# Performance work log

Hardware: AMD Instinct MI355X
Metric: run time of the kernel (lower is better)

The kernel has to match this reference:

```python
import jax, jax.numpy as jnp
import numpy as np

K = 5            # Chebyshev order (hard-coded in ManEmbedder conv_kwargs)
LAMBDA_MAX = 3.0 # fixed lambda_max from init
N_NODES = 100000
N_EDGES = 400000
N_GRAPHS = 64
H1, H2 = 128, 512


def _seg_sum(vals, idx, n):
    return jax.ops.segment_sum(vals, idx, num_segments=n)


def _cheb_edge_weights(edge_index, n_nodes):
    """Scaled Laplacian L_hat = 2*(I - D^-1/2 A D^-1/2)/lambda_max - I as edge weights.
    Matches PyG get_laplacian('sym') + ChebConv.__norm__ with fixed lambda_max.
    Degrees are computed at row = edge_index[0] (as in get_laplacian)."""
    row, col = edge_index[0], edge_index[1]
    ones = jnp.ones(row.shape[0], jnp.float32)
    deg = _seg_sum(ones, row, n_nodes)
    dinv = jnp.where(deg > 0, jax.lax.rsqrt(jnp.maximum(deg, 1e-12)), 0.0)
    w_edge = -(dinv[row] * dinv[col]) * (2.0 / LAMBDA_MAX)  # off-diagonal of L_hat
    w_loop = 2.0 / LAMBDA_MAX - 1.0                          # diagonal of L_hat (scalar)
    return w_edge, w_loop


def cheb_conv(x, edge_index, W, b, reverse):
    """PyG ChebConv. flow='target_to_source' (reverse=False): aggregate at row, gather at col.
    reverse=True flips the propagation direction (source_to_target)."""
    n = x.shape[0]
    w_edge, w_loop = _cheb_edge_weights(edge_index, n)
    row, col = edge_index[0], edge_index[1]
    src, dst = (row, col) if reverse else (col, row)

    def prop(h):  # L_hat @ h via gather-scale-scatter + diagonal term
        return _seg_sum(w_edge[:, None] * h[src], dst, n) + w_loop * h

    tx0 = x
    out = tx0 @ W[0]
    tx1 = prop(tx0)
    out = out + tx1 @ W[1]
    for k in range(2, K):
        tx2 = 2.0 * prop(tx1) - tx0
        out = out + tx2 @ W[k]
        tx0, tx1 = tx1, tx2
    return out + b


def bidir_block(x, edge_index, Wf, bf, Wb, bb):
    # Bidirectional: one ChebConv per edge direction, outputs summed.
    return cheb_conv(x, edge_index, Wf, bf, False) + cheb_conv(x, edge_index, Wb, bb, True)


def setup_inputs() -> dict:
    key = jax.random.key(0)
    ks = jax.random.split(key, 12)
    x = jax.random.normal(ks[0], (N_NODES, 1), jnp.float32)
    edge_index = jax.random.randint(ks[1], (2, N_EDGES), 0, N_NODES, dtype=jnp.int64)
    batch = jnp.sort(jax.random.randint(ks[2], (N_NODES,), 0, N_GRAPHS, dtype=jnp.int64))

    def glorot(k, shape):
        fan_in, fan_out = shape[-2], shape[-1]
        s = (6.0 / (fan_in + fan_out)) ** 0.5
        return jax.random.uniform(k, shape, jnp.float32, -s, s)

    return {
        "x": x, "edge_index": edge_index, "batch": batch,
        "W1f": glorot(ks[3], (K, 1, H1)),  "b1f": jnp.zeros((H1,), jnp.float32),
        "W1b": glorot(ks[4], (K, 1, H1)),  "b1b": jnp.zeros((H1,), jnp.float32),
        "W2f": glorot(ks[5], (K, H1, H2)), "b2f": jnp.zeros((H2,), jnp.float32),
        "W2b": glorot(ks[6], (K, H1, H2)), "b2b": jnp.zeros((H2,), jnp.float32),
    }


def reference(x, edge_index, batch, W1f, b1f, W1b, b1b, W2f, b2f, W2b, b2b):
    h = jax.nn.relu(bidir_block(x, edge_index, W1f, b1f, W1b, b1b))
    h = jax.nn.relu(bidir_block(h, edge_index, W2f, b2f, W2b, b2b))
    # global mean pool over batch index -> [N_GRAPHS, 512]
    summed = _seg_sum(h, batch, N_GRAPHS)
    counts = _seg_sum(jnp.ones((h.shape[0],), jnp.float32), batch, N_GRAPHS)
    return summed / jnp.maximum(counts, 1.0)[:, None]
```

## Files before the change

kernel.cpp:

```cpp
#include <hip/hip_runtime.h>
#include <hip/hip_bf16.h>

typedef unsigned short u16;
typedef unsigned int u32;
typedef __attribute__((ext_vector_type(4))) float f32x4;
typedef __attribute__((ext_vector_type(8))) short bf16x8;

struct __align__(8) ew_t { int s; float w; };

#define WLOOP (2.0f/3.0f - 1.0f)
#define WEDGE (-(2.0f/3.0f))

__device__ __forceinline__ float bf2f(u16 h){ u32 u = ((u32)h)<<16; float f; __builtin_memcpy(&f,&u,4); return f; }
__device__ __forceinline__ u16 f2bf(float f){ u32 u; __builtin_memcpy(&u,&f,4); u32 r = u + 0x7fffu + ((u>>16)&1u); return (u16)(r>>16); }

__device__ __forceinline__ void async16(u16* lds, const u16* g){
  __builtin_amdgcn_global_load_lds((const __attribute__((address_space(1))) u32*)g,
                                   (__attribute__((address_space(3))) u32*)lds, 16, 0, 0);
}

__global__ void k_hist(const int* __restrict__ ei, int E, int* cntf, int* cntb){
  int e = blockIdx.x*256 + threadIdx.x; if (e>=E) return;
  atomicAdd(&cntf[ei[e]],1); atomicAdd(&cntb[ei[E+e]],1);
}
__global__ void k_dinv(const int* __restrict__ cntf, float* dinv, int N){
  int n = blockIdx.x*256+threadIdx.x; if(n>=N) return;
  int d = cntf[n]; dinv[n] = d>0 ? rsqrtf((float)d) : 0.f;
}
__global__ void k_scanA(const int* __restrict__ cnt, int* excl, int* bsum, int n){
  __shared__ int sh[256]; int i = blockIdx.x*256+threadIdx.x;
  int v = (i<n)? cnt[i]:0; sh[threadIdx.x]=v; __syncthreads();
  for (int off=1; off<256; off<<=1){
    int t = (threadIdx.x>=off)? sh[threadIdx.x-off]:0; __syncthreads();
    sh[threadIdx.x]+=t; __syncthreads();
  }
  if (i<n) excl[i]=sh[threadIdx.x]-v;
  if (threadIdx.x==255) bsum[blockIdx.x]=sh[255];
}
__global__ void k_scanB(int* bsum, int nb, int* total){
  __shared__ int sh[512]; int t = threadIdx.x;
  int v = (t<nb)? bsum[t]:0; sh[t]=v; __syncthreads();
  for(int off=1; off<512; off<<=1){
    int a = (t>=off)? sh[t-off]:0; __syncthreads();
    sh[t]+=a; __syncthreads();
  }
  if (t<nb) bsum[t]=sh[t]-v;
  if (t==511) *total = sh[511];
}
__global__ void k_scanC(int* excl, const int* __restrict__ bsum, int n, int* cur){
  int i = blockIdx.x*256+threadIdx.x; if(i>=n) return;
  int v = excl[i]+bsum[blockIdx.x]; excl[i]=v; cur[i]=v;
}
__global__ void k_fill(const int* __restrict__ ei, int E, const float* __restrict__ dinv,
                       int* curf, int* curb, ew_t* ewf, ew_t* ewb){
  int e = blockIdx.x*256+threadIdx.x; if(e>=E) return;
  int r = ei[e], c = ei[E+e];
  float w = WEDGE * dinv[r]*dinv[c];
  int pf = atomicAdd(&curf[r],1); ewf[pf] = {c, w};
  int pb = atomicAdd(&curb[c],1); ewb[pb] = {r, w};
}

__global__ void k_sprop(const float* __restrict__ t1f, const float* __restrict__ t0f, float* df,
                        const float* __restrict__ t1b, const float* __restrict__ t0b, float* db,
                        const int* __restrict__ offf, const ew_t* __restrict__ ewfa,
                        const int* __restrict__ offb, const ew_t* __restrict__ ewba,
                        int N){
  int i = blockIdx.x*256+threadIdx.x;
  int dir = 0; if (i >= N){ i -= N; dir = 1; }
  if (i >= N) return;
  const float* t1; const float* t0; float* d; const int* off; const ew_t* ew;
  if (dir==0){ t1=t1f; t0=t0f; d=df; off=offf; ew=ewfa; }
  else       { t1=t1b; t0=t0b; d=db; off=offb; ew=ewba; }
  float a = WLOOP * t1[i];
  int e = off[i], e1 = off[i+1];
  for (; e+4<=e1; e+=4){
    ew_t p0=ew[e], p1=ew[e+1], p2=ew[e+2], p3=ew[e+3];
    float v0=t1[p0.s], v1=t1[p1.s], v2=t1[p2.s], v3=t1[p3.s];
    a += p0.w*v0 + p1.w*v1 + p2.w*v2 + p3.w*v3;
  }
  for (; e<e1; ++e){ ew_t p=ew[e]; a += p.w*t1[p.s]; }
  d[i] = t0 ? (2.f*a - t0[i]) : a;
}

__global__ void k_expand(const float* __restrict__ x,
   const float* __restrict__ cf1, const float* __restrict__ cf2, const float* __restrict__ cf3, const float* __restrict__ cf4,
   const float* __restrict__ cb1, const float* __restrict__ cb2, const float* __restrict__ cb3, const float* __restrict__ cb4,
   const float* __restrict__ W1f, const float* __restrict__ b1f,
   const float* __restrict__ W1b, const float* __restrict__ b1b,
   u16* __restrict__ T, int N){
  __shared__ float swf[640], swb[640], sbias[128];
  int tid = threadIdx.x;
  for (int i=tid;i<640;i+=256){ swf[i]=W1f[i]; swb[i]=W1b[i]; }
  if (tid<128) sbias[tid]=b1f[tid]+b1b[tid];
  __syncthreads();
  int j = tid & 127; int n = blockIdx.x*2 + (tid>>7);
  if (n>=N) return;
  float xx = x[n];
  float acc = sbias[j] + xx*(swf[j]+swb[j]);
  acc += cf1[n]*swf[128+j]; acc += cf2[n]*swf[256+j]; acc += cf3[n]*swf[384+j]; acc += cf4[n]*swf[512+j];
  acc += cb1[n]*swb[128+j]; acc += cb2[n]*swb[256+j]; acc += cb3[n]*swb[384+j]; acc += cb4[n]*swb[512+j];
  T[(size_t)n*1152 + j] = f2bf(fmaxf(acc,0.f));
}

__global__ void k_vprop(u16* __restrict__ T,
   const int* __restrict__ offf, const ew_t* __restrict__ ewfa,
   const int* __restrict__ offb, const ew_t* __restrict__ ewba,
   int ssf, int dsf, int psf, int ssb, int dsb, int psb, int N){
  int gid = blockIdx.x*256 + threadIdx.x;
  int wid = gid>>6, l = threadIdx.x & 63;
  int dir = 0; if (wid >= N){ wid -= N; dir = 1; }
  if (wid >= N) return;
  const int* off; const ew_t* ew; int ss,ds,ps;
  if (!dir){ off=offf;ew=ewfa;ss=ssf;ds=dsf;ps=psf; }
  else     { off=offb;ew=ewba;ss=ssb;ds=dsb;ps=psb; }
  const u16* Tss = T + (size_t)ss*128 + 2*l;
  u32 u = *(const u32*)(Tss + (size_t)wid*1152);
  float a0 = WLOOP*bf2f(u&0xffff), a1 = WLOOP*bf2f(u>>16);
  int e = off[wid], e1 = off[wid+1];
  for (; e+4<=e1; e+=4){
    ew_t p0=ew[e], p1=ew[e+1], p2=ew[e+2], p3=ew[e+3];
    u32 g0 = *(const u32*)(Tss + (size_t)p0.s*1152);
    u32 g1 = *(const u32*)(Tss + (size_t)p1.s*1152);
    u32 g2 = *(const u32*)(Tss + (size_t)p2.s*1152);
    u32 g3 = *(const u32*)(Tss + (size_t)p3.s*1152);
    a0 += p0.w*bf2f(g0&0xffff) + p1.w*bf2f(g1&0xffff) + p2.w*bf2f(g2&0xffff) + p3.w*bf2f(g3&0xffff);
    a1 += p0.w*bf2f(g0>>16)    + p1.w*bf2f(g1>>16)    + p2.w*bf2f(g2>>16)    + p3.w*bf2f(g3>>16);
  }
  for (; e<e1; ++e){
    ew_t p = ew[e];
    u32 ug = *(const u32*)(Tss + (size_t)p.s*1152);
    a0 += p.w*bf2f(ug&0xffff); a1 += p.w*bf2f(ug>>16);
  }
  float r0=a0, r1=a1;
  if (ps >= 0){
    u32 up = *(const u32*)(T + ((size_t)wid*1152 + ps*128) + 2*l);
    r0 = 2.f*a0 - bf2f(up&0xffff); r1 = 2.f*a1 - bf2f(up>>16);
  }
  *(u32*)(T + ((size_t)wid*1152 + ds*128) + 2*l) = ((u32)f2bf(r1)<<16) | (u32)f2bf(r0);
}

__global__ void k_wprep(const float* __restrict__ W2f, const float* __restrict__ W2b,
                        const float* __restrict__ b2f, const float* __restrict__ b2b,
                        u16* __restrict__ Wt2, float* __restrict__ bias2){
  int i = blockIdx.x*256+threadIdx.x;
  if (i < 512) bias2[i] = b2f[i]+b2b[i];
  if (i >= 512*1152) return;
  int j = i&7, l = (i>>3)&63, nt = (i>>9)&31, t = i>>14;
  int col = nt*16 + (l&15);
  int k   = t*32 + (l>>4)*8 + j;
  int s2 = k>>7, c = k&127;
  float v;
  if (s2==0)      v = W2f[c*512+col] + W2b[c*512+col];
  else if (s2<5)  v = W2f[(s2*128+c)*512 + col];
  else            v = W2b[((s2-4)*128+c)*512 + col];
  Wt2[i] = f2bf(v);
}

__global__ __launch_bounds__(512, 4) void k_gemm(const u16* __restrict__ T, const u16* __restrict__ Wt2,
                        const float* __restrict__ bias2, const int* __restrict__ batch,
                        float* __restrict__ outp, int Mvalid, int NB){
  int bid = blockIdx.x;
  int r8 = bid & 7, q = bid >> 3;
  int bn = q & 1, bm = (q >> 1)*8 + r8;
  if (bm >= NB) return;
  __shared__ u16 Al[2][128*32];
  int tid = threadIdx.x, w = tid>>6, l = tid&63;
  int wr = w>>2, wc = w&3;
  int hi = l>>4, lo = l&15;

  f32x4 acc[4][4];
  #pragma unroll
  for (int m=0;m<4;m++)
    #pragma unroll
    for (int n=0;n<4;n++){ acc[m][n][0]=0.f; acc[m][n][1]=0.f; acc[m][n][2]=0.f; acc[m][n][3]=0.f; }

  int sr = tid>>2, sp = tid&3;
  int csrc = ((sp ^ ((sr>>1)&3)))*8;
  const u16* asrc = T + (size_t)(bm*128 + sr)*1152 + csrc;
  const int adst = tid*8;
  int rsw = (hi ^ ((lo>>1)&3))*8;
  const int abase = (wr*64 + lo)*32 + rsw;
  const u16* bsrc = Wt2 + ((size_t)(bn*16 + wc*4)*64 + l)*8;

  #define LOADB(dst, t_) do { \
    _Pragma("unroll") \
    for (int n_=0;n_<4;n_++) dst[n_] = *(const bf16x8*)(bsrc + (size_t)(t_)*16384 + n_*512); \
  } while(0)

  bf16x8 be[4], bo[4];
  async16(&Al[0][adst], asrc);
  LOADB(be, 0);

  for (int t=0; t<36; t+=2){
    if (t < 35){
      async16(&Al[1][adst], asrc + (t+1)*32);
      LOADB(bo, t+1);
      asm volatile("s_waitcnt vmcnt(5)" ::: "memory");
    } else {
      asm volatile("s_waitcnt vmcnt(0)" ::: "memory");
    }
    asm volatile("s_barrier" ::: "memory");
    __builtin_amdgcn_s_setprio(1);
    #pragma unroll
    for (int m=0;m<4;m++){
      bf16x8 af = *(const bf16x8*)&Al[0][abase + m*512];
      #pragma unroll
      for (int n=0;n<4;n++)
        acc[m][n] = __builtin_amdgcn_mfma_f32_16x16x32_bf16(af, be[n], acc[m][n], 0, 0, 0);
    }
    __builtin_amdgcn_s_setprio(0);
    asm volatile("s_barrier" ::: "memory");
    if (t+2 < 36){
      async16(&Al[0][adst], asrc + (t+2)*32);
      LOADB(be, t+2);
      asm volatile("s_waitcnt vmcnt(5)" ::: "memory");
    } else {
      asm volatile("s_waitcnt vmcnt(0)" ::: "memory");
    }
    asm volatile("s_barrier" ::: "memory");
    __builtin_amdgcn_s_setprio(1);
    #pragma unroll
    for (int m=0;m<4;m++){
      bf16x8 af = *(const bf16x8*)&Al[1][abase + m*512];
      #pragma unroll
      for (int n=0;n<4;n++)
        acc[m][n] = __builtin_amdgcn_mfma_f32_16x16x32_bf16(af, bo[n], acc[m][n], 0, 0, 0);
    }
    __builtin_amdgcn_s_setprio(0);
    asm volatile("s_barrier" ::: "memory");
  }
  #undef LOADB

  int bg[16];
  #pragma unroll
  for (int m=0;m<4;m++)
    #pragma unroll
    for (int j2=0;j2<4;j2++){
      int row = bm*128 + wr*64 + m*16 + hi*4 + j2;
      bg[m*4+j2] = (row < Mvalid) ? batch[row] : -1;
    }
  #pragma unroll
  for (int n=0;n<4;n++){
    int col = bn*256 + wc*64 + n*16 + lo;
    float bc = bias2[col];
    int cg2 = -1; float ssum = 0.f;
    #pragma unroll
    for (int idx=0; idx<16; idx++){
      int g = bg[idx];
      if (g >= 0){
        float val = fmaxf(acc[idx>>2][n][idx&3] + bc, 0.f);
        if (g != cg2){ if (cg2 >= 0) atomicAdd(&outp[(cg2<<9) + col], ssum); cg2 = g; ssum = 0.f; }
        ssum += val;
      }
    }
    if (cg2 >= 0) atomicAdd(&outp[(cg2<<9) + col], ssum);
  }
}

__global__ void k_count(const int* __restrict__ batch, int* cg, int N){
  __shared__ int sh[64];
  int t = threadIdx.x;
  if (t < 64) sh[t] = 0;
  __syncthreads();
  int base = blockIdx.x*1024;
  #pragma unroll
  for (int i = base + t; i < base + 1024; i += 256){
    if (i < N) atomicAdd(&sh[batch[i]], 1);
  }
  __syncthreads();
  if (t < 64){ int v = sh[t]; if (v) atomicAdd(&cg[t], v); }
}

__global__ void k_div(float* out, const int* __restrict__ cg, int total){
  int i = blockIdx.x*256+threadIdx.x; if (i>=total) return;
  int g = i>>9; out[i] /= fmaxf((float)cg[g], 1.f);
}

extern "C" void kernel_launch(void* const* d_in, const int* in_sizes, int n_in,
                              void* d_out, int out_size, void* d_ws, size_t ws_size,
                              hipStream_t stream) {
  const float* x   = (const float*)d_in[0];
  const int*   ei  = (const int*)d_in[1];
  const int*   bat = (const int*)d_in[2];
  const float* W1f = (const float*)d_in[3];
  const float* b1f = (const float*)d_in[4];
  const float* W1b = (const float*)d_in[5];
  const float* b1b = (const float*)d_in[6];
  const float* W2f = (const float*)d_in[7];
  const float* b2f = (const float*)d_in[8];
  const float* W2b = (const float*)d_in[9];
  const float* b2b = (const float*)d_in[10];

  const int N  = in_sizes[0];
  const int E  = in_sizes[1] / 2;
  const int NP = ((N + 127)/128)*128;
  const int NB = NP/128;

  size_t p = 0;
  auto A = [&](size_t sz){ size_t r = p; p += (sz + 255) & ~(size_t)255; return r; };
  size_t o_cnt  = A(2*(size_t)N*4);
  size_t o_offf = A(((size_t)N+1)*4);
  size_t o_offb = A(((size_t)N+1)*4);
  size_t o_curf = A((size_t)N*4);
  size_t o_curb = A((size_t)N*4);
  size_t o_bsum = A(512*4);
  size_t o_dinv = A((size_t)N*4);
  size_t o_ewf  = A((size_t)E*8);
  size_t o_ewb  = A((size_t)E*8);
  size_t o_cf   = A(8*(size_t)N*4);
  size_t o_Wt   = A((size_t)512*1152*2);
  size_t o_b2   = A(512*4);
  size_t o_cg   = A(64*4);
  size_t o_T    = A((size_t)NP*1152*2);
  if (p > ws_size) return;

  char* ws = (char*)d_ws;
  int*   cnt_f = (int*)(ws + o_cnt);
  int*   cnt_b = cnt_f + N;
  int*   off_f = (int*)(ws + o_offf);
  int*   off_b = (int*)(ws + o_offb);
  int*   cur_f = (int*)(ws + o_curf);
  int*   cur_b = (int*)(ws + o_curb);
  int*   bsum  = (int*)(ws + o_bsum);
  float* dinv  = (float*)(ws + o_dinv);
  ew_t*  ewf   = (ew_t*)(ws + o_ewf);
  ew_t*  ewb   = (ew_t*)(ws + o_ewb);
  float* cf1   = (float*)(ws + o_cf);
  float* cf2   = cf1 + N; float* cf3 = cf2 + N; float* cf4 = cf3 + N;
  float* cb1   = cf4 + N; float* cb2 = cb1 + N; float* cb3 = cb2 + N; float* cb4 = cb3 + N;
  u16*   Wt2   = (u16*)(ws + o_Wt);
  float* bias2 = (float*)(ws + o_b2);
  int*   cg    = (int*)(ws + o_cg);
  u16*   T     = (u16*)(ws + o_T);
  float* outp  = (float*)d_out;

  const int nbN = (N + 255)/256;
  const int nbE = (E + 255)/256;
  const int nb2N = (2*N + 255)/256;

  hipMemsetAsync(cnt_f, 0, 2*(size_t)N*4, stream);
  hipMemsetAsync(cg, 0, 64*4, stream);
  hipMemsetAsync(d_out, 0, (size_t)out_size*4, stream);
  if (NP > N) hipMemsetAsync(T + (size_t)N*1152, 0, (size_t)(NP-N)*1152*2, stream);

  k_hist<<<nbE,256,0,stream>>>(ei, E, cnt_f, cnt_b);
  k_dinv<<<nbN,256,0,stream>>>(cnt_f, dinv, N);
  k_scanA<<<nbN,256,0,stream>>>(cnt_f, off_f, bsum, N);
  k_scanB<<<1,512,0,stream>>>(bsum, nbN, off_f + N);
  k_scanC<<<nbN,256,0,stream>>>(off_f, bsum, N, cur_f);
  k_scanA<<<nbN,256,0,stream>>>(cnt_b, off_b, bsum, N);
  k_scanB<<<1,512,0,stream>>>(bsum, nbN, off_b + N);
  k_scanC<<<nbN,256,0,stream>>>(off_b, bsum, N, cur_b);
  k_fill<<<nbE,256,0,stream>>>(ei, E, dinv, cur_f, cur_b, ewf, ewb);

  k_sprop<<<nb2N,256,0,stream>>>(x,   nullptr, cf1,  x,   nullptr, cb1, off_f,ewf, off_b,ewb, N);
  k_sprop<<<nb2N,256,0,stream>>>(cf1, x,       cf2,  cb1, x,       cb2, off_f,ewf, off_b,ewb, N);
  k_sprop<<<nb2N,256,0,stream>>>(cf2, cf1,     cf3,  cb2, cb1,     cb3, off_f,ewf, off_b,ewb, N);
  k_sprop<<<nb2N,256,0,stream>>>(cf3, cf2,     cf4,  cb3, cb2,     cb4, off_f,ewf, off_b,ewb, N);
  k_expand<<<(N+1)/2,256,0,stream>>>(x, cf1,cf2,cf3,cf4, cb1,cb2,cb3,cb4, W1f,b1f,W1b,b1b, T, N);

  k_wprep<<<(512*1152+255)/256,256,0,stream>>>(W2f, W2b, b2f, b2b, Wt2, bias2);

  const int vb = (2*N*64 + 255)/256;
  k_vprop<<<vb,256,0,stream>>>(T, off_f,ewf, off_b,ewb, 0,1,-1, 0,5,-1, N);
  k_vprop<<<vb,256,0,stream>>>(T, off_f,ewf, off_b,ewb, 1,2, 0, 5,6, 0, N);
  k_vprop<<<vb,256,0,stream>>>(T, off_f,ewf, off_b,ewb, 2,3, 1, 6,7, 5, N);
  k_vprop<<<vb,256,0,stream>>>(T, off_f,ewf, off_b,ewb, 3,4, 2, 7,8, 6, N);

  k_count<<<(N+1023)/1024,256,0,stream>>>(bat, cg, N);
  const int gemmGrid = ((NB + 7)/8)*8*2;
  k_gemm<<<gemmGrid,512,0,stream>>>(T, Wt2, bias2, bat, outp, N, NB);
  k_div<<<(out_size+255)/256,256,0,stream>>>(outp, cg, out_size);
}
```

Before: 639.8 us.

## Triple-buffer GEMM A tiles and predicate-unroll sparse propagation loops by eight

The GEMM main loop moves from a two-stage LDS ring to a three-stage ring, issuing the A-tile async load two steps ahead and the B register loads one step ahead, so each step needs one fewer wait on global memory. The scalar and vector sparse propagation kernels replace the 4-way unroll plus remainder loop with an 8-way unrolled loop whose tail lanes are masked by clamping the index and zeroing the weight. This puts more gathers in flight per node and removes the remainder loop, at the cost of redundant loads for masked lanes. The larger LDS footprint may lower GEMM occupancy.

Measured after the change: 700.9 us. 9.6% more time.

```diff
diff --git a/kernel.cpp b/kernel.cpp
--- a/kernel.cpp
+++ b/kernel.cpp
@@ -73,12 +73,14 @@
   else       { t1=t1b; t0=t0b; d=db; off=offb; ew=ewba; }
   float a = WLOOP * t1[i];
   int e = off[i], e1 = off[i+1];
-  for (; e+4<=e1; e+=4){
-    ew_t p0=ew[e], p1=ew[e+1], p2=ew[e+2], p3=ew[e+3];
-    float v0=t1[p0.s], v1=t1[p1.s], v2=t1[p2.s], v3=t1[p3.s];
-    a += p0.w*v0 + p1.w*v1 + p2.w*v2 + p3.w*v3;
-  }
-  for (; e<e1; ++e){ ew_t p=ew[e]; a += p.w*t1[p.s]; }
+  for (; e < e1; e += 8){
+    #pragma unroll
+    for (int j=0;j<8;j++){
+      int idx = e + j; bool v = idx < e1;
+      ew_t p = ew[v ? idx : e1-1];
+      a += (v ? p.w : 0.f) * t1[p.s];
+    }
+  }
   d[i] = t0 ? (2.f*a - t0[i]) : a;
 }
 
@@ -117,19 +119,16 @@
   u32 u = *(const u32*)(Tss + (size_t)wid*1152);
   float a0 = WLOOP*bf2f(u&0xffff), a1 = WLOOP*bf2f(u>>16);
   int e = off[wid], e1 = off[wid+1];
-  for (; e+4<=e1; e+=4){
-    ew_t p0=ew[e], p1=ew[e+1], p2=ew[e+2], p3=ew[e+3];
-    u32 g0 = *(const u32*)(Tss + (size_t)p0.s*1152);
-    u32 g1 = *(const u32*)(Tss + (size_t)p1.s*1152);
-    u32 g2 = *(const u32*)(Tss + (size_t)p2.s*1152);
-    u32 g3 = *(const u32*)(Tss + (size_t)p3.s*1152);
-    a0 += p0.w*bf2f(g0&0xffff) + p1.w*bf2f(g1&0xffff) + p2.w*bf2f(g2&0xffff) + p3.w*bf2f(g3&0xffff);
-    a1 += p0.w*bf2f(g0>>16)    + p1.w*bf2f(g1>>16)    + p2.w*bf2f(g2>>16)    + p3.w*bf2f(g3>>16);
-  }
-  for (; e<e1; ++e){
-    ew_t p = ew[e];
-    u32 ug = *(const u32*)(Tss + (size_t)p.s*1152);
-    a0 += p.w*bf2f(ug&0xffff); a1 += p.w*bf2f(ug>>16);
+  for (; e < e1; e += 8){
+    #pragma unroll
+    for (int j=0;j<8;j++){
+      int idx = e + j; bool v = idx < e1;
+      ew_t p = ew[v ? idx : e1-1];
+      float wj = v ? p.w : 0.f;
+      u32 g = *(const u32*)(Tss + (size_t)p.s*1152);
+      a0 += wj*bf2f(g&0xffff);
+      a1 += wj*bf2f(g>>16);
+    }
   }
   float r0=a0, r1=a1;
   if (ps >= 0){
@@ -163,7 +162,7 @@
   int r8 = bid & 7, q = bid >> 3;
   int bn = q & 1, bm = (q >> 1)*8 + r8;
   if (bm >= NB) return;
-  __shared__ u16 Al[2][128*32];
+  __shared__ u16 Al[3][128*32];
   int tid = threadIdx.x, w = tid>>6, l = tid&63;
   int wr = w>>2, wc = w&3;
   int hi = l>>4, lo = l&15;
@@ -190,45 +189,36 @@
   bf16x8 be[4], bo[4];
   async16(&Al[0][adst], asrc);
   LOADB(be, 0);
-
-  for (int t=0; t<36; t+=2){
-    if (t < 35){
-      async16(&Al[1][adst], asrc + (t+1)*32);
-      LOADB(bo, t+1);
-      asm volatile("s_waitcnt vmcnt(5)" ::: "memory");
-    } else {
-      asm volatile("s_waitcnt vmcnt(0)" ::: "memory");
-    }
-    asm volatile("s_barrier" ::: "memory");
-    __builtin_amdgcn_s_setprio(1);
-    #pragma unroll
-    for (int m=0;m<4;m++){
-      bf16x8 af = *(const bf16x8*)&Al[0][abase + m*512];
-      #pragma unroll
-      for (int n=0;n<4;n++)
-        acc[m][n] = __builtin_amdgcn_mfma_f32_16x16x32_bf16(af, be[n], acc[m][n], 0, 0, 0);
-    }
-    __builtin_amdgcn_s_setprio(0);
-    asm volatile("s_barrier" ::: "memory");
-    if (t+2 < 36){
-      async16(&Al[0][adst], asrc + (t+2)*32);
-      LOADB(be, t+2);
-      asm volatile("s_waitcnt vmcnt(5)" ::: "memory");
-    } else {
-      asm volatile("s_waitcnt vmcnt(0)" ::: "memory");
-    }
-    asm volatile("s_barrier" ::: "memory");
-    __builtin_amdgcn_s_setprio(1);
-    #pragma unroll
-    for (int m=0;m<4;m++){
-      bf16x8 af = *(const bf16x8*)&Al[1][abase + m*512];
-      #pragma unroll
-      for (int n=0;n<4;n++)
-        acc[m][n] = __builtin_amdgcn_mfma_f32_16x16x32_bf16(af, bo[n], acc[m][n], 0, 0, 0);
-    }
-    __builtin_amdgcn_s_setprio(0);
-    asm volatile("s_barrier" ::: "memory");
-  }
+  async16(&Al[1][adst], asrc + 32);
+
+  #define GSTEP(tc, bufC, bufS, BC, BN_) do { \
+    if ((tc)+1 < 36) LOADB(BN_, (tc)+1); \
+    if ((tc)+2 < 36) async16(&Al[bufS][adst], asrc + ((tc)+2)*32); \
+    if ((tc) < 34)      { asm volatile("s_waitcnt vmcnt(6)" ::: "memory"); } \
+    else if ((tc)==34)  { asm volatile("s_waitcnt vmcnt(5)" ::: "memory"); } \
+    else                { asm volatile("s_waitcnt vmcnt(0)" ::: "memory"); } \
+    asm volatile("s_barrier" ::: "memory"); \
+    __builtin_amdgcn_s_setprio(1); \
+    _Pragma("unroll") \
+    for (int m_=0;m_<4;m_++){ \
+      bf16x8 af = *(const bf16x8*)&Al[bufC][abase + m_*512]; \
+      _Pragma("unroll") \
+      for (int n_=0;n_<4;n_++) \
+        acc[m_][n_] = __builtin_amdgcn_mfma_f32_16x16x32_bf16(af, BC[n_], acc[m_][n_], 0, 0, 0); \
+    } \
+    __builtin_amdgcn_s_setprio(0); \
+    asm volatile("s_barrier" ::: "memory"); \
+  } while(0)
+
+  for (int t0=0; t0<36; t0+=6){
+    GSTEP(t0+0, 0, 2, be, bo);
+    GSTEP(t0+1, 1, 0, bo, be);
+    GSTEP(t0+2, 2, 1, be, bo);
+    GSTEP(t0+3, 0, 2, bo, be);
+    GSTEP(t0+4, 1, 0, be, bo);
+    GSTEP(t0+5, 2, 1, bo, be);
+  }
+  #undef GSTEP
   #undef LOADB
 
   int bg[16];
```
